# Kernel tuning notes

Measured on AMD Instinct MI355X. Metric: run time of the kernel, lower is better.

The kernel has to match this reference:

```python
import jax, jax.numpy as jnp
import numpy as np
from math import sqrt

B, IN_C, OUT_C, H, W, WDIM, K = 16, 512, 512, 64, 64, 512, 3
EPS = 1e-8
LRELU_SLOPE = 0.2


def setup_inputs() -> dict:
    key = jax.random.key(0)
    ks = jax.random.split(key, 5)
    return {
        "x": jax.random.normal(ks[0], (B, IN_C, H, W), dtype=jnp.float32),
        "w": jax.random.normal(ks[1], (B, WDIM), dtype=jnp.float32),
        "noise": jax.random.normal(ks[2], (B, 1, H, W), dtype=jnp.float32),
        "linear_w": jax.random.normal(ks[3], (IN_C, WDIM), dtype=jnp.float32),
        "linear_b": jnp.ones((IN_C,), dtype=jnp.float32),
        "conv_w": jax.random.normal(ks[4], (OUT_C, IN_C, K, K), dtype=jnp.float32),
        "scale_noise": jnp.zeros((OUT_C,), dtype=jnp.float32),
        "bias": jnp.zeros((OUT_C,), dtype=jnp.float32),
    }


def reference(x, w, noise, linear_w, linear_b, conv_w, scale_noise, bias):
    # EqualizerStraights: equalized-lr linear, scale = 1/sqrt(w_dim)
    s = w @ (linear_w * (1.0 / sqrt(WDIM))).T + linear_b  # [b, in_c]
    # Weight_Demod: equalized conv weight, scale = 1/sqrt(in_c*k*k)
    base_w = conv_w * (1.0 / sqrt(IN_C * K * K))  # [out, in, k, k]
    weights = base_w[None] * s[:, None, :, None, None]  # [b, out, in, k, k]
    sigma_inv = jax.lax.rsqrt(
        jnp.sum(weights * weights, axis=(2, 3, 4), keepdims=True) + EPS)
    weights = weights * sigma_inv

    def conv1(xi, wi):  # xi [in,h,w], wi [out,in,k,k]
        return jax.lax.conv_general_dilated(
            xi[None], wi, window_strides=(1, 1), padding="SAME",
            dimension_numbers=("NCHW", "OIHW", "NCHW"))[0]

    y = jax.vmap(conv1)(x, weights)  # [b, out, h, w]
    y = y + scale_noise[None, :, None, None] * noise
    return jax.nn.leaky_relu(y + bias[None, :, None, None], negative_slope=LRELU_SLOPE)
```

## Files before the change

kernel.cpp:

```cpp
#include <hip/hip_runtime.h>
#include <hip/hip_bf16.h>
#include <stdint.h>

typedef __bf16 bf16_t;
typedef __bf16 bf16x8 __attribute__((ext_vector_type(8)));
typedef short short8 __attribute__((ext_vector_type(8)));
typedef float f32x4 __attribute__((ext_vector_type(4)));

#define RS512  0.044194173824159216f
#define RS4608 0.014731391274719739f

__global__ void k_style(const float* __restrict__ w, const float* __restrict__ lw,
                        const float* __restrict__ lb, float* __restrict__ s) {
  int b = blockIdx.y;
  int c = blockIdx.x * 256 + threadIdx.x;
  const float4* wr = (const float4*)(w + b * 512);
  const float4* lr = (const float4*)(lw + (size_t)c * 512);
  float acc = 0.f;
#pragma unroll 4
  for (int d = 0; d < 128; ++d) {
    float4 a = wr[d], q = lr[d];
    acc += a.x * q.x + a.y * q.y + a.z * q.z + a.w * q.w;
  }
  s[b * 512 + c] = acc * RS512 + lb[c];
}

__global__ void k_wprep(const float* __restrict__ cw, float* __restrict__ wsq,
                        bf16_t* __restrict__ bwf) {
  int idx = blockIdx.x * 256 + threadIdx.x;
  int o = idx >> 9, i = idx & 511;
  float v[9];
  float ss = 0.f;
#pragma unroll
  for (int t = 0; t < 9; ++t) {
    float x = cw[(size_t)idx * 9 + t] * RS4608;
    v[t] = x;
    ss += x * x;
  }
  wsq[idx] = ss;
  int lane = (o & 15) | (((i >> 3) & 3) << 4);
  int base_blk = (i >> 5) * 32 + (o >> 4);
#pragma unroll
  for (int t = 0; t < 9; ++t) {
    size_t e = ((size_t)(t * 512 + base_blk) << 9) + lane * 8 + (i & 7);
    bwf[e] = (bf16_t)v[t];
  }
}

__global__ void k_sigma(const float* __restrict__ s, const float* __restrict__ wsq,
                        float* __restrict__ sinv) {
  __shared__ float s2[512];
  int b = blockIdx.y;
  int o = blockIdx.x * 256 + threadIdx.x;
  for (int i = threadIdx.x; i < 512; i += 256) {
    float v = s[b * 512 + i];
    s2[i] = v * v;
  }
  __syncthreads();
  const float4* qr = (const float4*)(wsq + (size_t)o * 512);
  float acc = 0.f;
#pragma unroll 4
  for (int d = 0; d < 128; ++d) {
    float4 q = qr[d];
    acc += q.x * s2[4 * d] + q.y * s2[4 * d + 1] + q.z * s2[4 * d + 2] + q.w * s2[4 * d + 3];
  }
  sinv[b * 512 + o] = rsqrtf(acc + 1e-8f);
}

__global__ void k_xt(const float* __restrict__ x, const float* __restrict__ s,
                     bf16_t* __restrict__ xt) {
  int ic = blockIdx.x, h = blockIdx.y, b = blockIdx.z;
  __shared__ __align__(16) bf16_t tile[8192];
  int t = threadIdx.x;
  int wcol = t & 63;
  int g = t >> 6;
#pragma unroll
  for (int blk = 0; blk < 4; ++blk) {
    int grp = blk * 4 + g;
    bf16x8 vec;
#pragma unroll
    for (int k = 0; k < 8; ++k) {
      int i = ic * 128 + grp * 8 + k;
      float v = x[(((size_t)b * 512 + i) * 64 + h) * 64 + wcol] * s[b * 512 + i];
      vec[k] = (bf16_t)v;
    }
    int chunk = grp ^ (wcol & 15);
    *(bf16x8*)((char*)tile + wcol * 256 + chunk * 16) = vec;
  }
  __syncthreads();
#pragma unroll
  for (int j = 0; j < 4; ++j) {
    int flat = j * 256 + t;
    int wo = flat >> 4, ig8 = flat & 15;
    int chunk = ig8 ^ (wo & 15);
    bf16x8 v = *(bf16x8*)((char*)tile + wo * 256 + chunk * 16);
    int c32 = (ig8 >> 2);
    int slot = (ig8 & 3) ^ ((wo >> 1) & 3);
    *(bf16x8*)(xt + (((size_t)b * 64 + h) * 64 + wo) * 512 + ic * 128 + c32 * 32 + slot * 8) = v;
  }
}

#define AS1 __attribute__((address_space(1)))
#define AS3 __attribute__((address_space(3)))

__device__ __forceinline__ void gl16(const void* g, void* l) {
  __builtin_amdgcn_global_load_lds((const AS1 void*)g, (AS3 void*)l, 16, 0, 0);
}

#define VMCNT(n) asm volatile("s_waitcnt vmcnt(" #n ")" ::: "memory")

__global__ __launch_bounds__(256, 2) void k_conv(
    const bf16_t* __restrict__ xt, const bf16_t* __restrict__ bwf,
    const float* __restrict__ sinv, const float* __restrict__ noise,
    const float* __restrict__ snz, const float* __restrict__ bias,
    float* __restrict__ out) {
  __shared__ __align__(16) char lds[77824];

  const int t = threadIdx.x;
  const int rq = blockIdx.x;
  const int oy = blockIdx.y;
  const int b = blockIdx.z;
  const int h0 = rq * 4;
  const int lane = t & 63;
  const int wv = t >> 6;
  const int wm = wv >> 1;
  const int wn = wv & 1;

  const bf16_t* xb = xt + (size_t)b * 2097152;
  const bf16_t* wsrc = bwf + (((size_t)(oy * 8 + wv * 2)) << 9) + lane * 8;

  f32x4 acc[4][8] = {};

  auto stageXrow = [&](int c, int buf, int r) {
    int gr = h0 - 1 + r;
    if ((unsigned)gr < 64u) {
      gl16(xb + (size_t)gr * 32768 + (size_t)(t >> 2) * 512 + c * 32 + (t & 3) * 8,
           lds + buf * 24576 + r * 4096 + (wv << 10));
    } else {
      gl16(xb + (size_t)(t >> 2) * 512 + c * 32 + (t & 3) * 8, lds + 73728 + (wv << 10));
    }
  };

  auto stageW = [&](int cc, int tt, int buf) {
    const bf16_t* s0 = wsrc + (size_t)(tt * 16 + cc) * 16384;
    char* d0 = lds + 49152 + buf * 8192 + (wv << 11);
    gl16(s0, d0);
    gl16(s0 + 512, d0 + 1024);
  };

  auto compute_tap = [&](int xbuf, int tap) {
    const int ky = tap / 3, kx = tap % 3;
    const char* wb = lds + 49152 + (tap % 3) * 8192 + (wm << 12) + (lane << 4);
    bf16x8 af[4];
#pragma unroll
    for (int mi = 0; mi < 4; ++mi) af[mi] = *(const bf16x8*)(wb + mi * 1024);
    bf16x8 bfr[8];
#pragma unroll
    for (int ni = 0; ni < 8; ++ni) {
      const int rslot = wn * 2 + (ni >> 2) + ky;
      int icol = (ni & 3) * 16 + (lane & 15) + kx - 1;
      bool valid = (unsigned)icol < 64u;
      int ic2 = valid ? icol : 0;
      int slot = (lane >> 4) ^ ((ic2 >> 1) & 3);
      short8 xv = *(const short8*)(lds + xbuf * 24576 + rslot * 4096 + ic2 * 64 + slot * 16);
      if (!valid) xv = (short8)0;
      bfr[ni] = __builtin_bit_cast(bf16x8, xv);
    }
    __builtin_amdgcn_s_setprio(1);
#pragma unroll
    for (int mi = 0; mi < 4; ++mi)
#pragma unroll
      for (int ni = 0; ni < 8; ++ni)
        acc[mi][ni] =
            __builtin_amdgcn_mfma_f32_16x16x32_bf16(af[mi], bfr[ni], acc[mi][ni], 0, 0, 0);
    __builtin_amdgcn_s_setprio(0);
  };

#define PHASE(c, tp, LAST)                                                     \
  {                                                                            \
    if (!(LAST) && (tp) < 6) stageXrow((c) + 1, (((c)&1) ^ 1), (tp));          \
    if (!(LAST) || (tp) <= 6) {                                                \
      if ((tp) + 2 <= 8) stageW((c), (tp) + 2, ((tp) + 2) % 3);                \
      else stageW((c) + 1, (tp) - 7, ((tp) + 2) % 3);                          \
    }                                                                          \
    if (LAST) {                                                                \
      if ((tp) <= 6) { VMCNT(4); }                                             \
      else if ((tp) == 7) { VMCNT(2); }                                        \
      else { VMCNT(0); }                                                       \
    } else {                                                                   \
      if ((tp) == 0 || (tp) == 6) { VMCNT(5); }                                \
      else if ((tp) <= 5) { VMCNT(6); }                                        \
      else { VMCNT(4); }                                                       \
    }                                                                          \
    __builtin_amdgcn_s_barrier();                                              \
    compute_tap((c) & 1, (tp));                                                \
  }

  if (h0 == 0) {
    *(f32x4*)(lds + t * 16) = (f32x4)0.f;
    *(f32x4*)(lds + 24576 + t * 16) = (f32x4)0.f;
  }
  if (h0 == 60) {
    *(f32x4*)(lds + 5 * 4096 + t * 16) = (f32x4)0.f;
    *(f32x4*)(lds + 24576 + 5 * 4096 + t * 16) = (f32x4)0.f;
  }
  asm volatile("s_waitcnt lgkmcnt(0)" ::: "memory");
#pragma unroll
  for (int r = 0; r < 6; ++r) stageXrow(0, 0, r);
  stageW(0, 0, 0);
  stageW(0, 1, 1);

  for (int c = 0; c < 15; ++c) {
#pragma unroll
    for (int tp = 0; tp < 9; ++tp) PHASE(c, tp, 0);
  }
#pragma unroll
  for (int tp = 0; tp < 9; ++tp) PHASE(15, tp, 1);

  const float* sb = sinv + b * 512;
  const int og = oy * 128 + wm * 64 + ((lane >> 4) << 2);
  const int colb = lane & 15;
  float nzv[8];
#pragma unroll
  for (int ni = 0; ni < 8; ++ni) {
    int prow = h0 + wn * 2 + (ni >> 2);
    int col = (ni & 3) * 16 + colb;
    nzv[ni] = noise[(size_t)b * 4096 + prow * 64 + col];
  }
#pragma unroll
  for (int mi = 0; mi < 4; ++mi) {
#pragma unroll
    for (int r = 0; r < 4; ++r) {
      int o = og + mi * 16 + r;
      float sv = sb[o];
      float nw = snz[o];
      float bv = bias[o];
      float* obase = out + ((size_t)b * 512 + o) * 4096;
#pragma unroll
      for (int ni = 0; ni < 8; ++ni) {
        int prow = h0 + wn * 2 + (ni >> 2);
        int col = (ni & 3) * 16 + colb;
        float v = acc[mi][ni][r] * sv + nw * nzv[ni] + bv;
        obase[prow * 64 + col] = v > 0.f ? v : 0.2f * v;
      }
    }
  }
}

extern "C" void kernel_launch(void* const* d_in, const int* in_sizes, int n_in,
                              void* d_out, int out_size, void* d_ws, size_t ws_size,
                              hipStream_t stream) {
  const float* x     = (const float*)d_in[0];
  const float* w     = (const float*)d_in[1];
  const float* noise = (const float*)d_in[2];
  const float* lw    = (const float*)d_in[3];
  const float* lb    = (const float*)d_in[4];
  const float* cw    = (const float*)d_in[5];
  const float* snz   = (const float*)d_in[6];
  const float* bias  = (const float*)d_in[7];
  float* out = (float*)d_out;

  char* ws = (char*)d_ws;
  bf16_t* xt   = (bf16_t*)ws;
  bf16_t* bwf  = (bf16_t*)(ws + 67108864);
  float*  s    = (float*)(ws + 71827456);
  float*  sinv = (float*)(ws + 71860224);
  float*  wsq  = (float*)(ws + 71892992);

  k_style<<<dim3(2, 16), 256, 0, stream>>>(w, lw, lb, s);
  k_wprep<<<dim3(1024), 256, 0, stream>>>(cw, wsq, bwf);
  k_sigma<<<dim3(2, 16), 256, 0, stream>>>(s, wsq, sinv);
  k_xt<<<dim3(4, 64, 16), 256, 0, stream>>>(x, s, xt);
  k_conv<<<dim3(16, 4, 16), 256, 0, stream>>>(xt, bwf, sinv, noise, snz, bias, out);
}
```

Measured before the change: 300.7 us.

## Reuse loaded input row across kx taps via DPP lane rotations

Input fragments are read from LDS only once per row (at kx==0) and kept in registers. The kx shifts are built with DPP row rotations plus a boundary select from the neighbouring fragment. This removes two of every three LDS reads of the activation tile and the per-element bounds checks. In exchange it adds DPP moves and selects, keeps 32 extra VGPRs live across taps, and depends on the taps running in kx order within one row.

```diff
diff --git a/kernel.cpp b/kernel.cpp
--- a/kernel.cpp
+++ b/kernel.cpp
@@ -6,6 +6,7 @@
 typedef __bf16 bf16x8 __attribute__((ext_vector_type(8)));
 typedef short short8 __attribute__((ext_vector_type(8)));
 typedef float f32x4 __attribute__((ext_vector_type(4)));
+typedef int int4v __attribute__((ext_vector_type(4)));
 
 #define RS512  0.044194173824159216f
 #define RS4608 0.014731391274719739f
@@ -109,6 +110,31 @@
 
 #define VMCNT(n) asm volatile("s_waitcnt vmcnt(" #n ")" ::: "memory")
 
+__device__ __forceinline__ int4v dpp_ror1(int4v v) {
+  int4v r;
+  r[0] = __builtin_amdgcn_mov_dpp(v[0], 0x121, 0xf, 0xf, true);
+  r[1] = __builtin_amdgcn_mov_dpp(v[1], 0x121, 0xf, 0xf, true);
+  r[2] = __builtin_amdgcn_mov_dpp(v[2], 0x121, 0xf, 0xf, true);
+  r[3] = __builtin_amdgcn_mov_dpp(v[3], 0x121, 0xf, 0xf, true);
+  return r;
+}
+__device__ __forceinline__ int4v dpp_rol1(int4v v) {
+  int4v r;
+  r[0] = __builtin_amdgcn_mov_dpp(v[0], 0x12F, 0xf, 0xf, true);
+  r[1] = __builtin_amdgcn_mov_dpp(v[1], 0x12F, 0xf, 0xf, true);
+  r[2] = __builtin_amdgcn_mov_dpp(v[2], 0x12F, 0xf, 0xf, true);
+  r[3] = __builtin_amdgcn_mov_dpp(v[3], 0x12F, 0xf, 0xf, true);
+  return r;
+}
+__device__ __forceinline__ int4v sel4(bool c, int4v a, int4v b) {
+  int4v r;
+  r[0] = c ? a[0] : b[0];
+  r[1] = c ? a[1] : b[1];
+  r[2] = c ? a[2] : b[2];
+  r[3] = c ? a[3] : b[3];
+  return r;
+}
+
 __global__ __launch_bounds__(256, 2) void k_conv(
     const bf16_t* __restrict__ xt, const bf16_t* __restrict__ bwf,
     const float* __restrict__ sinv, const float* __restrict__ noise,
@@ -130,6 +156,9 @@
   const bf16_t* wsrc = bwf + (((size_t)(oy * 8 + wv * 2)) << 9) + lane * 8;
 
   f32x4 acc[4][8] = {};
+  int4v F[8];
+  const bool c0 = (lane & 15) == 0;
+  const bool c15 = (lane & 15) == 15;
 
   auto stageXrow = [&](int c, int buf, int r) {
     int gr = h0 - 1 + r;
@@ -150,29 +179,50 @@
 
   auto compute_tap = [&](int xbuf, int tap) {
     const int ky = tap / 3, kx = tap % 3;
-    const char* wb = lds + 49152 + (tap % 3) * 8192 + (wm << 12) + (lane << 4);
+    const char* wbse = lds + 49152 + (tap % 3) * 8192 + (wm << 12) + (lane << 4);
     bf16x8 af[4];
 #pragma unroll
-    for (int mi = 0; mi < 4; ++mi) af[mi] = *(const bf16x8*)(wb + mi * 1024);
-    bf16x8 bfr[8];
-#pragma unroll
-    for (int ni = 0; ni < 8; ++ni) {
-      const int rslot = wn * 2 + (ni >> 2) + ky;
-      int icol = (ni & 3) * 16 + (lane & 15) + kx - 1;
-      bool valid = (unsigned)icol < 64u;
-      int ic2 = valid ? icol : 0;
-      int slot = (lane >> 4) ^ ((ic2 >> 1) & 3);
-      short8 xv = *(const short8*)(lds + xbuf * 24576 + rslot * 4096 + ic2 * 64 + slot * 16);
-      if (!valid) xv = (short8)0;
-      bfr[ni] = __builtin_bit_cast(bf16x8, xv);
+    for (int mi = 0; mi < 4; ++mi) af[mi] = *(const bf16x8*)(wbse + mi * 1024);
+
+    __builtin_amdgcn_s_setprio(1);
+    if (kx == 0) {
+#pragma unroll
+      for (int ni = 0; ni < 8; ++ni) {
+        const int rslot = wn * 2 + (ni >> 2) + ky;
+        const int icol = (ni & 3) * 16 + (lane & 15);
+        const int slot = (lane >> 4) ^ ((icol >> 1) & 3);
+        F[ni] = *(const int4v*)(lds + xbuf * 24576 + rslot * 4096 + icol * 64 + slot * 16);
+      }
+#pragma unroll
+      for (int ni = 0; ni < 8; ++ni) {
+        int4v g = dpp_ror1(F[ni]);
+        int4v p = ((ni & 3) == 0) ? (int4v)0 : dpp_ror1(F[ni - 1]);
+        int4v bv = sel4(c0, p, g);
+#pragma unroll
+        for (int mi = 0; mi < 4; ++mi)
+          acc[mi][ni] = __builtin_amdgcn_mfma_f32_16x16x32_bf16(
+              af[mi], __builtin_bit_cast(bf16x8, bv), acc[mi][ni], 0, 0, 0);
+      }
+    } else if (kx == 1) {
+#pragma unroll
+      for (int ni = 0; ni < 8; ++ni) {
+#pragma unroll
+        for (int mi = 0; mi < 4; ++mi)
+          acc[mi][ni] = __builtin_amdgcn_mfma_f32_16x16x32_bf16(
+              af[mi], __builtin_bit_cast(bf16x8, F[ni]), acc[mi][ni], 0, 0, 0);
+      }
+    } else {
+#pragma unroll
+      for (int ni = 0; ni < 8; ++ni) {
+        int4v g = dpp_rol1(F[ni]);
+        int4v p = ((ni & 3) == 3) ? (int4v)0 : dpp_rol1(F[ni + 1]);
+        int4v bv = sel4(c15, p, g);
+#pragma unroll
+        for (int mi = 0; mi < 4; ++mi)
+          acc[mi][ni] = __builtin_amdgcn_mfma_f32_16x16x32_bf16(
+              af[mi], __builtin_bit_cast(bf16x8, bv), acc[mi][ni], 0, 0, 0);
+      }
     }
-    __builtin_amdgcn_s_setprio(1);
-#pragma unroll
-    for (int mi = 0; mi < 4; ++mi)
-#pragma unroll
-      for (int ni = 0; ni < 8; ++ni)
-        acc[mi][ni] =
-            __builtin_amdgcn_mfma_f32_16x16x32_bf16(af[mi], bfr[ni], acc[mi][ni], 0, 0, 0);
     __builtin_amdgcn_s_setprio(0);
   };
 
```

Result: no change. 304.9 us (+1.4%).
